# Optimization experiments

Hardware: AMD Instinct MI355X
Metric: run time of the kernel (lower is better)

## Reference

```python
import jax, jax.numpy as jnp
import numpy as np

TEMPERATURE = 1.0          # max(args.matching_temperature=1.0, 1e-6)
CONSISTENCY_WEIGHT = 0.5   # max(args.matching_consistency_weight=0.5, 0.0)
EPS = 1e-6

N, M, D, K = 16384, 16384, 128, 5


def setup_inputs() -> dict:
    key = jax.random.key(0)
    k1, k2, k3 = jax.random.split(key, 3)
    query = jax.random.normal(k1, (N, D), dtype=jnp.float32)
    memory_bank = jax.random.normal(k2, (M, D), dtype=jnp.float32)
    # per-memory-entry neighbor scale (positive), as in _build_patch_library_statistics
    neighbor_scale_bank = jax.random.uniform(k3, (M,), dtype=jnp.float32) + 0.1
    return {"query": query, "memory_bank": memory_bank,
            "neighbor_scale_bank": neighbor_scale_bank, "k": K}


def reference(query, memory_bank, neighbor_scale_bank, k):
    # Euclidean cdist: [N, M]
    q2 = jnp.sum(query * query, axis=-1, keepdims=True)            # [N,1]
    m2 = jnp.sum(memory_bank * memory_bank, axis=-1)               # [M]
    d2 = q2 + m2 - 2.0 * (query @ memory_bank.T)                   # [N,M]
    dist = jnp.sqrt(jnp.maximum(d2, 1e-12))

    # torch.topk(largest=False) -> k smallest distances, ascending
    neg_d, knn_indices = jax.lax.top_k(-dist, k)                   # [N,k]
    knn_distances = -neg_d

    # adaptive_knn reduction (_reduce_knn_distances)
    weights = jax.nn.softmax(-knn_distances / TEMPERATURE, axis=1)
    weighted_distance = jnp.sum(weights * knn_distances, axis=1)   # [N]

    neighbor_scale = jnp.mean(neighbor_scale_bank[knn_indices], axis=1)  # [N]
    normalized_distance = weighted_distance / jnp.maximum(neighbor_scale, EPS)

    mean_d = jnp.mean(knn_distances, axis=1)
    std_d = jnp.sqrt(jnp.maximum(
        jnp.mean((knn_distances - mean_d[:, None]) ** 2, axis=1), 0.0))  # unbiased=False
    consistency = std_d / jnp.maximum(mean_d, EPS)

    return normalized_distance * (1.0 + CONSISTENCY_WEIGHT * consistency)
```

## Files before the change

kernel.cpp:

```cpp
#include <hip/hip_runtime.h>
#include <hip/hip_bf16.h>
#include <math.h>

#define N_Q 16384
#define N_M 16384
#define DIM 128
#define KNN 5
#define SPLITS 8
#define COLS_PER_SPLIT (N_M / SPLITS)
#define ITERS (COLS_PER_SPLIT / 128)
#define BROWS 256
#define TSEL 8
#define LLIST 4
#define BIGF 3.0e38f

typedef __bf16 bf16x8 __attribute__((ext_vector_type(8)));
typedef float f32x4 __attribute__((ext_vector_type(4)));

__device__ __forceinline__ void gl2lds16(const void* g, void* l) {
    __builtin_amdgcn_global_load_lds(
        (const __attribute__((address_space(1))) void*)g,
        (__attribute__((address_space(3))) void*)l, 16, 0, 0);
}

__device__ __forceinline__ unsigned umed3(unsigned a, unsigned b, unsigned c) {
    unsigned d;
    asm("v_med3_u32 %0, %1, %2, %3" : "=v"(d) : "v"(a), "v"(b), "v"(c));
    return d;
}

template <int D>
__device__ __forceinline__ void insD(unsigned (&L)[D], unsigned k) {
#pragma unroll
    for (int i = D - 1; i >= 1; --i) L[i] = umed3(L[i - 1], L[i], k);
    L[0] = min(L[0], k);
}

__global__ void prep_kernel(const float* __restrict__ q,
                            const float* __restrict__ mem,
                            float* __restrict__ q2, float* __restrict__ m2,
                            float* __restrict__ m2b,
                            __hip_bfloat16* __restrict__ qb,
                            __hip_bfloat16* __restrict__ mb) {
    int gt = blockIdx.x * blockDim.x + threadIdx.x;
    int wid = gt >> 6;
    int lane = gt & 63;
    bool isq = wid < N_Q;
    int r = isq ? wid : wid - N_Q;
    const float* src = (isq ? q : mem) + (size_t)r * DIM;
    __hip_bfloat16* bdst = (isq ? qb : mb) + (size_t)r * DIM;
    float2 v = reinterpret_cast<const float2*>(src)[lane];
    float sc = isq ? 1.0f : -2.0f;
    __hip_bfloat162 bv;
    bv.x = __float2bfloat16(sc * v.x);
    bv.y = __float2bfloat16(sc * v.y);
    reinterpret_cast<__hip_bfloat162*>(bdst)[lane] = bv;
    float s = fmaf(v.x, v.x, v.y * v.y);
#pragma unroll
    for (int off = 32; off > 0; off >>= 1) s += __shfl_down(s, off, 64);
    if (lane == 0) {
        if (isq) {
            q2[r] = s;
        } else {
            m2[r] = s;
            m2b[r] = s + 256.0f;
        }
    }
}

__device__ __forceinline__ void mfma_chunk(const unsigned char* cbuf,
                                           int lds_base,
                                           const bf16x8 (&afrag)[4][4],
                                           const float (&m2r)[8], int c,
                                           f32x4 (&acc)[4][2]) {
#pragma unroll
    for (int ti = 0; ti < 4; ++ti)
#pragma unroll
        for (int c2 = 0; c2 < 2; ++c2) {
            float m = m2r[c * 2 + c2];
            acc[ti][c2] = (f32x4){m, m, m, m};
        }
#pragma unroll
    for (int ks = 0; ks < 4; ++ks) {
        const unsigned char* bp =
            cbuf + (lds_base ^ (ks << 6)) + (c >> 1) * 16384;
#pragma unroll
        for (int c2 = 0; c2 < 2; ++c2) {
            bf16x8 bfr = *reinterpret_cast<const bf16x8*>(
                bp + ((c & 1) * 2 + c2) * 4096);
#pragma unroll
            for (int ti = 0; ti < 4; ++ti)
                acc[ti][c2] = __builtin_amdgcn_mfma_f32_16x16x32_bf16(
                    afrag[ti][ks], bfr, acc[ti][c2], 0, 0, 0);
        }
    }
}

__device__ __forceinline__ void select_chunk(unsigned (&lst)[16][LLIST],
                                             const f32x4 (&acc)[4][2],
                                             unsigned cv0, unsigned cv1) {
#pragma unroll
    for (int ti = 0; ti < 4; ++ti)
#pragma unroll
        for (int r = 0; r < 4; ++r) {
            const int rr = ti * 4 + r;
            insD(lst[rr], (__float_as_uint(acc[ti][0][r]) & 0xFFFFC000u) | cv0);
            insD(lst[rr], (__float_as_uint(acc[ti][1][r]) & 0xFFFFC000u) | cv1);
        }
}

__global__ __launch_bounds__(256, 2) void knn_tops_kernel(
    const __hip_bfloat16* __restrict__ qb, const __hip_bfloat16* __restrict__ mb,
    const float* __restrict__ m2b, unsigned* __restrict__ candK) {
    __shared__ __align__(16) unsigned char smem[65536];
    const int tid = threadIdx.x;
    const int w = tid >> 6;
    const int lane = tid & 63;
    const int i16 = lane & 15;
    const int g = lane >> 4;
    const int row0 = blockIdx.x * BROWS;
    const int col0 = blockIdx.y * COLS_PER_SPLIT;

    bf16x8 afrag[4][4];
#pragma unroll
    for (int ti = 0; ti < 4; ++ti) {
        const __hip_bfloat16* qrow =
            qb + (size_t)(row0 + w * 64 + ti * 16 + i16) * DIM;
#pragma unroll
        for (int ks = 0; ks < 4; ++ks)
            afrag[ti][ks] = *reinterpret_cast<const bf16x8*>(qrow + ks * 32 + g * 8);
    }

    unsigned lst[16][LLIST];
#pragma unroll
    for (int rr = 0; rr < 16; ++rr)
#pragma unroll
        for (int j = 0; j < LLIST; ++j) lst[rr][j] = 0xFFFFFFFFu;

    const int lds_base = i16 * 256 + ((g ^ (i16 & 7)) << 4);
    int soff[8];
#pragma unroll
    for (int it = 0; it < 8; ++it) {
        int fg = w * 512 + it * 64 + lane;
        int c = fg >> 4, sg = fg & 15;
        int gk = (sg & 8) | ((sg ^ c) & 7);
        soff[it] = c * DIM + gk * 8;
    }
    const __hip_bfloat16* mbt = mb + (size_t)col0 * DIM;

    f32x4 accA[4][2], accB[4][2];
#pragma unroll
    for (int ti = 0; ti < 4; ++ti)
#pragma unroll
        for (int c2 = 0; c2 < 2; ++c2)
            accB[ti][c2] = (f32x4){BIGF, BIGF, BIGF, BIGF};
    unsigned pcv0 = 0, pcv1 = 0;

#pragma unroll
    for (int it = 0; it < 8; ++it)
        gl2lds16(mbt + soff[it], smem + w * 8192 + it * 1024);
    mbt += 128 * DIM;

    for (int t = 0; t < ITERS; ++t) {
        __syncthreads();
        const unsigned char* cbuf = smem + ((t & 1) << 15);
        if (t + 1 < ITERS) {
            unsigned char* nbuf = smem + (((t + 1) & 1) << 15);
#pragma unroll
            for (int it = 0; it < 8; ++it)
                gl2lds16(mbt + soff[it], nbuf + w * 8192 + it * 1024);
            mbt += 128 * DIM;
        }

        float m2r[8];
        unsigned colv[8];
#pragma unroll
        for (int cg = 0; cg < 8; ++cg) {
            int cl = col0 + t * 128 + cg * 16 + i16;
            m2r[cg] = m2b[cl];
            colv[cg] = (unsigned)cl;
        }

        mfma_chunk(cbuf, lds_base, afrag, m2r, 0, accA);
        select_chunk(lst, accB, pcv0, pcv1);
        mfma_chunk(cbuf, lds_base, afrag, m2r, 1, accB);
        select_chunk(lst, accA, colv[0], colv[1]);
        mfma_chunk(cbuf, lds_base, afrag, m2r, 2, accA);
        select_chunk(lst, accB, colv[2], colv[3]);
        mfma_chunk(cbuf, lds_base, afrag, m2r, 3, accB);
        select_chunk(lst, accA, colv[4], colv[5]);
        pcv0 = colv[6];
        pcv1 = colv[7];
    }
    select_chunk(lst, accB, pcv0, pcv1);

    __syncthreads();

#pragma unroll
    for (int rr = 0; rr < 16; ++rr) {
        unsigned pv[LLIST];
#pragma unroll
        for (int j = 0; j < LLIST; ++j)
            pv[j] = (unsigned)__shfl_xor((int)lst[rr][j], 8, 64);
#pragma unroll
        for (int j = 0; j < LLIST; ++j) insD(lst[rr], pv[j]);
    }
    unsigned* MG = (unsigned*)smem;
    if (i16 < 8) {
#pragma unroll
        for (int rr = 0; rr < 16; ++rr) {
            int row = w * 64 + (rr >> 2) * 16 + g * 4 + (rr & 3);
#pragma unroll
            for (int j = 0; j < LLIST; ++j)
                MG[row * 33 + i16 * LLIST + j] = lst[rr][j];
        }
    }
    __syncthreads();
    {
        unsigned bk[TSEL];
#pragma unroll
        for (int j = 0; j < TSEL; ++j) bk[j] = 0xFFFFFFFFu;
        for (int c = 0; c < 32; ++c) {
            unsigned k = MG[tid * 33 + c];
            insD(bk, k);
        }
        size_t base = (size_t)(row0 + tid) * (SPLITS * TSEL) + blockIdx.y * TSEL;
        *reinterpret_cast<uint4*>(candK + base) =
            make_uint4(bk[0], bk[1], bk[2], bk[3]);
        *reinterpret_cast<uint4*>(candK + base + 4) =
            make_uint4(bk[4], bk[5], bk[6], bk[7]);
    }
}

__global__ __launch_bounds__(256) void finalize_kernel(
    const float* __restrict__ q, const float* __restrict__ mem,
    const float* __restrict__ q2, const float* __restrict__ m2,
    const unsigned* __restrict__ candK, const float* __restrict__ scaleb,
    float* __restrict__ out) {
    int wv = threadIdx.x >> 6, lane = threadIdx.x & 63;
    int n = blockIdx.x * 4 + wv;

    unsigned v64 = candK[(size_t)n * (SPLITS * TSEL) + lane];
#pragma unroll
    for (int k = 2; k <= 64; k <<= 1) {
#pragma unroll
        for (int j = k >> 1; j > 0; j >>= 1) {
            unsigned ov = (unsigned)__shfl_xor((int)v64, j, 64);
            unsigned mn = min(v64, ov), mx = max(v64, ov);
            bool up = ((lane & k) == 0);
            v64 = (((lane & j) == 0) == up) ? mn : mx;
        }
    }
    int cand = lane >> 2, qd = lane & 3;
    int ci = (int)((unsigned)__shfl((int)v64, cand, 64) & 0x3FFFu);

    const float4* qr = reinterpret_cast<const float4*>(q + (size_t)n * DIM) + qd * 8;
    const float4* mr = reinterpret_cast<const float4*>(mem + (size_t)ci * DIM) + qd * 8;
    float dot = 0.f;
#pragma unroll
    for (int k = 0; k < 8; ++k) {
        float4 a = qr[k], b = mr[k];
        dot = fmaf(a.x, b.x, fmaf(a.y, b.y, fmaf(a.z, b.z, fmaf(a.w, b.w, dot))));
    }
    dot += __shfl_xor(dot, 1, 64);
    dot += __shfl_xor(dot, 2, 64);
    float v = (qd == 0) ? (q2[n] + m2[ci] - 2.f * dot) : BIGF;

    float dk[KNN]; int ik[KNN];
#pragma unroll
    for (int r = 0; r < KNN; ++r) {
        float mv = v; int ml = lane;
#pragma unroll
        for (int off = 32; off > 0; off >>= 1) {
            float ov = __shfl_xor(mv, off, 64);
            int   ol = __shfl_xor(ml, off, 64);
            if (ov < mv || (ov == mv && ol < ml)) { mv = ov; ml = ol; }
        }
        dk[r] = sqrtf(fmaxf(mv, 1e-12f));
        ik[r] = __shfl(ci, ml, 64);
        if (lane == ml) v = BIGF;
    }
    if (lane == 0) {
        float dmin = dk[0];
        float se = 0.f, wd = 0.f, sm = 0.f, ssc = 0.f;
#pragma unroll
        for (int j = 0; j < KNN; ++j) {
            float e = expf(-(dk[j] - dmin));
            se += e;
            wd = fmaf(e, dk[j], wd);
            sm += dk[j];
            ssc += scaleb[ik[j]];
        }
        wd /= se;
        float scale = ssc * 0.2f;
        float nd = wd / fmaxf(scale, 1e-6f);
        float mean = sm * 0.2f;
        float var = 0.f;
#pragma unroll
        for (int j = 0; j < KNN; ++j) {
            float dd = dk[j] - mean;
            var = fmaf(dd, dd, var);
        }
        var *= 0.2f;
        float cons = sqrtf(var) / fmaxf(mean, 1e-6f);
        out[n] = nd * (1.f + 0.5f * cons);
    }
}

extern "C" void kernel_launch(void* const* d_in, const int* in_sizes, int n_in,
                              void* d_out, int out_size, void* d_ws,
                              size_t ws_size, hipStream_t stream) {
    const float* query  = (const float*)d_in[0];
    const float* mem    = (const float*)d_in[1];
    const float* scaleb = (const float*)d_in[2];
    float* out = (float*)d_out;

    float* q2 = (float*)d_ws;
    float* m2 = q2 + N_Q;
    float* m2b = m2 + N_M;
    __hip_bfloat16* qb = (__hip_bfloat16*)(m2b + N_M);
    __hip_bfloat16* mb = qb + (size_t)N_Q * DIM;
    unsigned* candK = (unsigned*)(mb + (size_t)N_M * DIM);

    prep_kernel<<<(N_Q + N_M) / 4, 256, 0, stream>>>(query, mem, q2, m2, m2b,
                                                     qb, mb);
    dim3 gridB(N_Q / BROWS, SPLITS);
    knn_tops_kernel<<<gridB, 256, 0, stream>>>(qb, mb, m2b, candK);
    finalize_kernel<<<N_Q / 4, 256, 0, stream>>>(query, mem, q2, m2, candK,
                                                 scaleb, out);
}
```

Measured before the change: 189.2 us.

## Fuse finalize into knn kernel via last-block atomic counter per row tile

```diff
diff --git a/kernel.cpp b/kernel.cpp
--- a/kernel.cpp
+++ b/kernel.cpp
@@ -41,7 +41,9 @@
                             float* __restrict__ q2, float* __restrict__ m2,
                             float* __restrict__ m2b,
                             __hip_bfloat16* __restrict__ qb,
-                            __hip_bfloat16* __restrict__ mb) {
+                            __hip_bfloat16* __restrict__ mb,
+                            unsigned* __restrict__ cnt) {
+    if (blockIdx.x == 0 && threadIdx.x < 64) cnt[threadIdx.x] = 0;
     int gt = blockIdx.x * blockDim.x + threadIdx.x;
     int wid = gt >> 6;
     int lane = gt & 63;
@@ -110,8 +112,12 @@
 }
 
 __global__ __launch_bounds__(256, 2) void knn_tops_kernel(
+    const float* __restrict__ q, const float* __restrict__ mem,
     const __hip_bfloat16* __restrict__ qb, const __hip_bfloat16* __restrict__ mb,
-    const float* __restrict__ m2b, unsigned* __restrict__ candK) {
+    const float* __restrict__ m2b, const float* __restrict__ q2,
+    const float* __restrict__ m2, const float* __restrict__ scaleb,
+    unsigned* __restrict__ candK, unsigned* __restrict__ cnt,
+    float* __restrict__ out) {
     __shared__ __align__(16) unsigned char smem[65536];
     const int tid = threadIdx.x;
     const int w = tid >> 6;
@@ -230,80 +236,87 @@
         *reinterpret_cast<uint4*>(candK + base + 4) =
             make_uint4(bk[4], bk[5], bk[6], bk[7]);
     }
-}
-
-__global__ __launch_bounds__(256) void finalize_kernel(
-    const float* __restrict__ q, const float* __restrict__ mem,
-    const float* __restrict__ q2, const float* __restrict__ m2,
-    const unsigned* __restrict__ candK, const float* __restrict__ scaleb,
-    float* __restrict__ out) {
-    int wv = threadIdx.x >> 6, lane = threadIdx.x & 63;
-    int n = blockIdx.x * 4 + wv;
-
-    unsigned v64 = candK[(size_t)n * (SPLITS * TSEL) + lane];
-#pragma unroll
-    for (int k = 2; k <= 64; k <<= 1) {
-#pragma unroll
-        for (int j = k >> 1; j > 0; j >>= 1) {
-            unsigned ov = (unsigned)__shfl_xor((int)v64, j, 64);
-            unsigned mn = min(v64, ov), mx = max(v64, ov);
-            bool up = ((lane & k) == 0);
-            v64 = (((lane & j) == 0) == up) ? mn : mx;
-        }
-    }
-    int cand = lane >> 2, qd = lane & 3;
-    int ci = (int)((unsigned)__shfl((int)v64, cand, 64) & 0x3FFFu);
-
-    const float4* qr = reinterpret_cast<const float4*>(q + (size_t)n * DIM) + qd * 8;
-    const float4* mr = reinterpret_cast<const float4*>(mem + (size_t)ci * DIM) + qd * 8;
-    float dot = 0.f;
-#pragma unroll
-    for (int k = 0; k < 8; ++k) {
-        float4 a = qr[k], b = mr[k];
-        dot = fmaf(a.x, b.x, fmaf(a.y, b.y, fmaf(a.z, b.z, fmaf(a.w, b.w, dot))));
-    }
-    dot += __shfl_xor(dot, 1, 64);
-    dot += __shfl_xor(dot, 2, 64);
-    float v = (qd == 0) ? (q2[n] + m2[ci] - 2.f * dot) : BIGF;
-
-    float dk[KNN]; int ik[KNN];
-#pragma unroll
-    for (int r = 0; r < KNN; ++r) {
-        float mv = v; int ml = lane;
-#pragma unroll
-        for (int off = 32; off > 0; off >>= 1) {
-            float ov = __shfl_xor(mv, off, 64);
-            int   ol = __shfl_xor(ml, off, 64);
-            if (ov < mv || (ov == mv && ol < ml)) { mv = ov; ml = ol; }
-        }
-        dk[r] = sqrtf(fmaxf(mv, 1e-12f));
-        ik[r] = __shfl(ci, ml, 64);
-        if (lane == ml) v = BIGF;
-    }
-    if (lane == 0) {
-        float dmin = dk[0];
-        float se = 0.f, wd = 0.f, sm = 0.f, ssc = 0.f;
-#pragma unroll
-        for (int j = 0; j < KNN; ++j) {
-            float e = expf(-(dk[j] - dmin));
-            se += e;
-            wd = fmaf(e, dk[j], wd);
-            sm += dk[j];
-            ssc += scaleb[ik[j]];
-        }
-        wd /= se;
-        float scale = ssc * 0.2f;
-        float nd = wd / fmaxf(scale, 1e-6f);
-        float mean = sm * 0.2f;
-        float var = 0.f;
-#pragma unroll
-        for (int j = 0; j < KNN; ++j) {
-            float dd = dk[j] - mean;
-            var = fmaf(dd, dd, var);
-        }
-        var *= 0.2f;
-        float cons = sqrtf(var) / fmaxf(mean, 1e-6f);
-        out[n] = nd * (1.f + 0.5f * cons);
+
+    __threadfence();
+    __syncthreads();
+    if (tid == 0)
+        *(unsigned*)smem = atomicAdd(&cnt[blockIdx.x], 1u);
+    __syncthreads();
+    if (*(unsigned*)smem != SPLITS - 1) return;
+    __threadfence();
+
+    for (int qi = 0; qi < 64; ++qi) {
+        int n = row0 + w * 64 + qi;
+        unsigned v64 = candK[(size_t)n * (SPLITS * TSEL) + lane];
+#pragma unroll
+        for (int k = 2; k <= 64; k <<= 1) {
+#pragma unroll
+            for (int j = k >> 1; j > 0; j >>= 1) {
+                unsigned ov = (unsigned)__shfl_xor((int)v64, j, 64);
+                unsigned mn = min(v64, ov), mx = max(v64, ov);
+                bool up = ((lane & k) == 0);
+                v64 = (((lane & j) == 0) == up) ? mn : mx;
+            }
+        }
+        int cand = lane >> 2, qd = lane & 3;
+        int ci = (int)((unsigned)__shfl((int)v64, cand, 64) & 0x3FFFu);
+
+        const float4* qr =
+            reinterpret_cast<const float4*>(q + (size_t)n * DIM) + qd * 8;
+        const float4* mr =
+            reinterpret_cast<const float4*>(mem + (size_t)ci * DIM) + qd * 8;
+        float dot = 0.f;
+#pragma unroll
+        for (int k = 0; k < 8; ++k) {
+            float4 a = qr[k], b = mr[k];
+            dot = fmaf(a.x, b.x,
+                       fmaf(a.y, b.y, fmaf(a.z, b.z, fmaf(a.w, b.w, dot))));
+        }
+        dot += __shfl_xor(dot, 1, 64);
+        dot += __shfl_xor(dot, 2, 64);
+        float v = (qd == 0) ? (q2[n] + m2[ci] - 2.f * dot) : BIGF;
+
+        float dk[KNN];
+        int ik[KNN];
+#pragma unroll
+        for (int r = 0; r < KNN; ++r) {
+            float mv = v;
+            int ml = lane;
+#pragma unroll
+            for (int off = 32; off > 0; off >>= 1) {
+                float ov = __shfl_xor(mv, off, 64);
+                int ol = __shfl_xor(ml, off, 64);
+                if (ov < mv || (ov == mv && ol < ml)) { mv = ov; ml = ol; }
+            }
+            dk[r] = sqrtf(fmaxf(mv, 1e-12f));
+            ik[r] = __shfl(ci, ml, 64);
+            if (lane == ml) v = BIGF;
+        }
+        if (lane == 0) {
+            float dmin = dk[0];
+            float se = 0.f, wd = 0.f, sm = 0.f, ssc = 0.f;
+#pragma unroll
+            for (int j = 0; j < KNN; ++j) {
+                float e = expf(-(dk[j] - dmin));
+                se += e;
+                wd = fmaf(e, dk[j], wd);
+                sm += dk[j];
+                ssc += scaleb[ik[j]];
+            }
+            wd /= se;
+            float scale = ssc * 0.2f;
+            float nd = wd / fmaxf(scale, 1e-6f);
+            float mean = sm * 0.2f;
+            float var = 0.f;
+#pragma unroll
+            for (int j = 0; j < KNN; ++j) {
+                float dd = dk[j] - mean;
+                var = fmaf(dd, dd, var);
+            }
+            var *= 0.2f;
+            float cons = sqrtf(var) / fmaxf(mean, 1e-6f);
+            out[n] = nd * (1.f + 0.5f * cons);
+        }
     }
 }
 
@@ -321,11 +334,11 @@
     __hip_bfloat16* qb = (__hip_bfloat16*)(m2b + N_M);
     __hip_bfloat16* mb = qb + (size_t)N_Q * DIM;
     unsigned* candK = (unsigned*)(mb + (size_t)N_M * DIM);
+    unsigned* cnt = candK + (size_t)N_Q * SPLITS * TSEL;
 
     prep_kernel<<<(N_Q + N_M) / 4, 256, 0, stream>>>(query, mem, q2, m2, m2b,
-                                                     qb, mb);
+                                                     qb, mb, cnt);
     dim3 gridB(N_Q / BROWS, SPLITS);
-    knn_tops_kernel<<<gridB, 256, 0, stream>>>(qb, mb, m2b, candK);
-    finalize_kernel<<<N_Q / 4, 256, 0, stream>>>(query, mem, q2, m2, candK,
-                                                 scaleb, out);
-}
+    knn_tops_kernel<<<gridB, 256, 0, stream>>>(query, mem, qb, mb, m2b, q2, m2,
+                                               scaleb, candK, cnt, out);
+}
```

Result: slower. 619.7 us (+227.6%).
